# Kernel tuning notes

Measured on AMD Instinct MI355X. Metric: run time of the kernel, lower is better.

The kernel has to match this reference:

```python
import jax, jax.numpy as jnp
import numpy as np

ALPHA = 1.702
LIMIT = 7.0


def setup_inputs() -> dict:
    key = jax.random.key(0)
    ks = jax.random.split(key, 6)
    T, H, D, E = 8192, 1024, 1024, 8
    hidden_states = jax.random.normal(ks[0], (T, H), dtype=jnp.float32)
    routing_weights = jax.random.uniform(ks[1], (T, E), dtype=jnp.float32)
    # 0.02 scale keeps activations in a sane range (original uses raw randn params)
    gate_up_proj = jax.random.normal(ks[2], (E, H, 2 * D), dtype=jnp.float32) * 0.02
    gate_up_proj_bias = jax.random.normal(ks[3], (E, 2 * D), dtype=jnp.float32) * 0.02
    down_proj = jax.random.normal(ks[4], (E, D, H), dtype=jnp.float32) * 0.02
    down_proj_bias = jax.random.normal(ks[5], (E, H), dtype=jnp.float32) * 0.02
    return {
        "hidden_states": hidden_states,
        "routing_weights": routing_weights,
        "gate_up_proj": gate_up_proj,
        "gate_up_proj_bias": gate_up_proj_bias,
        "down_proj": down_proj,
        "down_proj_bias": down_proj_bias,
    }


def reference(hidden_states, routing_weights, gate_up_proj, gate_up_proj_bias,
              down_proj, down_proj_bias):
    # hidden_states: [T, H]; routing_weights: [T, E] (batch_size == T in the torch code)
    B, H = hidden_states.shape[0], hidden_states.shape[-1]
    hs = hidden_states.reshape(-1, H)  # [T, H]
    # all-experts batched GEMM: [E, T, 2D]
    gate_up = jnp.einsum('th,ehd->etd', hs, gate_up_proj) + gate_up_proj_bias[:, None, :]
    gate = jnp.minimum(gate_up[..., ::2], LIMIT)          # [E, T, D]
    up = jnp.clip(gate_up[..., 1::2], -LIMIT, LIMIT)      # [E, T, D]
    glu = gate * jax.nn.sigmoid(gate * ALPHA)
    # down projection: [E, T, H]
    next_states = jnp.einsum('etd,edh->eth', (up + 1.0) * glu, down_proj) \
        + down_proj_bias[:, None, :]
    # routing-weighted combine over experts: [T, H]
    out = jnp.einsum('eth,te->th', next_states, routing_weights)
    return out.reshape(B, -1, H)  # [T, 1, H], matching final .view(batch_size, -1, hidden)
```

## Files before the change

### kernel.cpp

```cpp
#include <hip/hip_runtime.h>
#include <hip/hip_bf16.h>

#define T_DIM 8192
#define H_DIM 1024
#define D_DIM 1024
#define E_DIM 8
#define TWO_D 2048
#define K2 8192

#define ALPHA_C 1.702f
#define LIMIT_C 7.0f

typedef __attribute__((ext_vector_type(8))) short s8v;
typedef __attribute__((ext_vector_type(4))) float f4v;

__device__ __forceinline__ void g2l16(const void* g, void* l) {
    __builtin_amdgcn_global_load_lds((const __attribute__((address_space(1))) void*)g,
                                     (__attribute__((address_space(3))) void*)l, 16, 0, 0);
}

__device__ __forceinline__ unsigned short f2bf(float f) {
    __hip_bfloat16 h = __float2bfloat16(f);
    return __builtin_bit_cast(unsigned short, h);
}

__device__ __forceinline__ float bf2f(unsigned short u) {
    unsigned int x = ((unsigned int)u) << 16;
    return __builtin_bit_cast(float, x);
}


__global__ void f32_to_bf16_kernel(const float* __restrict__ in,
                                   unsigned short* __restrict__ out, size_t n) {
    size_t i = ((size_t)blockIdx.x * blockDim.x + threadIdx.x) * 4;
    if (i + 3 < n) {
        float4 v = *(const float4*)(in + i);
        ushort4 o;
        o.x = f2bf(v.x); o.y = f2bf(v.y); o.z = f2bf(v.z); o.w = f2bf(v.w);
        *(ushort4*)(out + i) = o;
    }
}

__global__ void transpose_conv_kernel(const float* __restrict__ in,
                                      unsigned short* __restrict__ out,
                                      int cols, size_t ibs, size_t obs, size_t ors,
                                      int remap) {
    __shared__ float t[32][33];
    const int b = blockIdx.z;
    const int c0 = blockIdx.x * 32, r0 = blockIdx.y * 32;
    const int tx = threadIdx.x & 31, ty = threadIdx.x >> 5;
    const float* ip = in + (size_t)b * ibs;
    #pragma unroll
    for (int i = 0; i < 4; ++i)
        t[ty + i * 8][tx] = ip[(size_t)(r0 + ty + i * 8) * cols + c0 + tx];
    __syncthreads();
    unsigned short* op = out + (size_t)b * obs;
    #pragma unroll
    for (int i = 0; i < 4; ++i) {
        int c = c0 + ty + i * 8;
        int nc = remap ? ((c & ~31) + ((c & 1) << 4) + ((c >> 1) & 15)) : c;
        op[(size_t)nc * ors + r0 + tx] = f2bf(t[tx][ty + i * 8]);
    }
}

__global__ void reduce_bias_kernel(const unsigned short* __restrict__ p0,
                                   const unsigned short* __restrict__ p1,
                                   const unsigned short* __restrict__ p2,
                                   const float* __restrict__ rw,
                                   const float* __restrict__ b3,
                                   float* __restrict__ out) {
    const int t = blockIdx.x;
    const int h = threadIdx.x * 4;
    const size_t idx = (size_t)t * H_DIM + h;
    float r[E_DIM];
    #pragma unroll
    for (int e = 0; e < E_DIM; ++e) r[e] = rw[(size_t)t * E_DIM + e];
    float4 v = *(const float4*)(out + idx);
    ushort4 a = *(const ushort4*)(p0 + idx);
    ushort4 b = *(const ushort4*)(p1 + idx);
    ushort4 c = *(const ushort4*)(p2 + idx);
    v.x += bf2f(a.x) + bf2f(b.x) + bf2f(c.x);
    v.y += bf2f(a.y) + bf2f(b.y) + bf2f(c.y);
    v.z += bf2f(a.z) + bf2f(b.z) + bf2f(c.z);
    v.w += bf2f(a.w) + bf2f(b.w) + bf2f(c.w);
    #pragma unroll
    for (int e = 0; e < E_DIM; ++e) {
        float4 bb = *(const float4*)(b3 + (size_t)e * H_DIM + h);
        v.x += r[e] * bb.x; v.y += r[e] * bb.y; v.z += r[e] * bb.z; v.w += r[e] * bb.w;
    }
    *(float4*)(out + idx) = v;
}


__global__ __launch_bounds__(256, 2) void gemm1_kernel(
    const short* __restrict__ Ag0,
    const short* __restrict__ Bg0,
    const float* __restrict__ b1,
    const float* __restrict__ rw,
    __hip_bfloat16* __restrict__ act2)
{
    const int e = blockIdx.z;
    const int mBase = blockIdx.x * 128;
    const int nBase = blockIdx.y * 128;
    const int tid = threadIdx.x;
    const int lane = tid & 63;
    const int wave = tid >> 6;
    const int wm = wave >> 1, wn = wave & 1;
    const int cq = lane & 15, quad = lane >> 4;

    __shared__ __align__(16) short As[128 * 64];
    __shared__ __align__(16) short Bs[128 * 64];

    const short* Ag = Ag0 + (size_t)mBase * H_DIM;
    const short* Bg = Bg0 + ((size_t)e * TWO_D + nBase) * H_DIM;

    f4v acc[4][4];
    #pragma unroll
    for (int mt = 0; mt < 4; ++mt)
        #pragma unroll
        for (int nt = 0; nt < 4; ++nt)
            acc[mt][nt] = (f4v){0.f, 0.f, 0.f, 0.f};

    const int srow8 = lane >> 3;
    const int gco = ((lane & 7) ^ srow8) * 8;
    const int cq7 = cq & 7;

    for (int k0 = 0; k0 < H_DIM; k0 += 64) {
        #pragma unroll
        for (int i = 0; i < 4; ++i) {
            const int r = wave * 32 + i * 8 + srow8;
            g2l16(Ag + (size_t)r * H_DIM + k0 + gco, As + (wave * 32 + i * 8) * 64);
            g2l16(Bg + (size_t)r * H_DIM + k0 + gco, Bs + (wave * 32 + i * 8) * 64);
        }
        __syncthreads();
        #pragma unroll
        for (int h = 0; h < 2; ++h) {
            s8v af[4], bf[4];
            const int pc = (((h << 2) + quad) ^ cq7) * 8;
            #pragma unroll
            for (int i = 0; i < 4; ++i) {
                af[i] = *(const s8v*)(As + (wm * 64 + i * 16 + cq) * 64 + pc);
                bf[i] = *(const s8v*)(Bs + (wn * 64 + i * 16 + cq) * 64 + pc);
            }
            #pragma unroll
            for (int mt = 0; mt < 4; ++mt)
                #pragma unroll
                for (int nt = 0; nt < 4; ++nt)
                    acc[mt][nt] = __builtin_amdgcn_mfma_f32_16x16x32_bf16(
                        af[mt], bf[nt], acc[mt][nt], 0, 0, 0);
        }
        __syncthreads();
    }

    float rwv[4][4];
    #pragma unroll
    for (int mt = 0; mt < 4; ++mt)
        #pragma unroll
        for (int r = 0; r < 4; ++r)
            rwv[mt][r] = rw[(size_t)(mBase + wm * 64 + mt * 16 + quad * 4 + r) * E_DIM + e];

    #pragma unroll
    for (int p = 0; p < 2; ++p) {
        const int j = (((nBase + wn * 64 + p * 32) >> 5) << 4) + cq;
        const float gb = b1[(size_t)e * TWO_D + 2 * j];
        const float ub = b1[(size_t)e * TWO_D + 2 * j + 1];
        #pragma unroll
        for (int mt = 0; mt < 4; ++mt) {
            #pragma unroll
            for (int r = 0; r < 4; ++r) {
                float gate = acc[mt][2 * p][r] + gb;
                float up   = acc[mt][2 * p + 1][r] + ub;
                gate = fminf(gate, LIMIT_C);
                up = fminf(fmaxf(up, -LIMIT_C), LIMIT_C);
                float glu = gate / (1.f + __expf(-ALPHA_C * gate));
                float a = (up + 1.f) * glu * rwv[mt][r];
                const int row = mBase + wm * 64 + mt * 16 + quad * 4 + r;
                act2[(size_t)row * K2 + (size_t)e * D_DIM + j] = __float2bfloat16(a);
            }
        }
    }
}


#define KSLICE 2048

__global__ __launch_bounds__(256, 2) void gemm2_kernel(
    const short* __restrict__ Ag0,
    const short* __restrict__ Bg0,
    float* __restrict__ out,
    unsigned short* __restrict__ p0,
    unsigned short* __restrict__ p1,
    unsigned short* __restrict__ p2)
{
    const int id = blockIdx.x;
    const int nBase = (id & 7) * 128;
    const int mBase = ((id >> 3) & 63) * 128;
    const int kIdx = id >> 9;
    const int kBase = kIdx * KSLICE;
    const int tid = threadIdx.x;
    const int lane = tid & 63;
    const int wave = tid >> 6;
    const int wm = wave >> 1, wn = wave & 1;
    const int cq = lane & 15, quad = lane >> 4;

    __shared__ __align__(16) short As[128 * 64];
    __shared__ __align__(16) short Bs[128 * 64];

    const short* Ag = Ag0 + (size_t)mBase * K2;
    const short* Bg = Bg0 + (size_t)nBase * K2;

    f4v acc[4][4];
    #pragma unroll
    for (int mt = 0; mt < 4; ++mt)
        #pragma unroll
        for (int nt = 0; nt < 4; ++nt)
            acc[mt][nt] = (f4v){0.f, 0.f, 0.f, 0.f};

    const int srow8 = lane >> 3;
    const int gco = ((lane & 7) ^ srow8) * 8;
    const int cq7 = cq & 7;

    for (int k0 = kBase; k0 < kBase + KSLICE; k0 += 64) {
        #pragma unroll
        for (int i = 0; i < 4; ++i) {
            const int r = wave * 32 + i * 8 + srow8;
            g2l16(Ag + (size_t)r * K2 + k0 + gco, As + (wave * 32 + i * 8) * 64);
            g2l16(Bg + (size_t)r * K2 + k0 + gco, Bs + (wave * 32 + i * 8) * 64);
        }
        __syncthreads();
        #pragma unroll
        for (int h = 0; h < 2; ++h) {
            s8v af[4], bf[4];
            const int pc = (((h << 2) + quad) ^ cq7) * 8;
            #pragma unroll
            for (int i = 0; i < 4; ++i) {
                af[i] = *(const s8v*)(As + (wm * 64 + i * 16 + cq) * 64 + pc);
                bf[i] = *(const s8v*)(Bs + (wn * 64 + i * 16 + cq) * 64 + pc);
            }
            #pragma unroll
            for (int mt = 0; mt < 4; ++mt)
                #pragma unroll
                for (int nt = 0; nt < 4; ++nt)
                    acc[mt][nt] = __builtin_amdgcn_mfma_f32_16x16x32_bf16(
                        af[mt], bf[nt], acc[mt][nt], 0, 0, 0);
        }
        __syncthreads();
    }

    unsigned short* pdst = (kIdx == 1) ? p0 : (kIdx == 2) ? p1 : p2;
    #pragma unroll
    for (int mt = 0; mt < 4; ++mt) {
        #pragma unroll
        for (int r = 0; r < 4; ++r) {
            const int row = mBase + wm * 64 + mt * 16 + quad * 4 + r;
            const size_t idx = (size_t)row * H_DIM + nBase + wn * 64 + 16 * 0 + cq;
            #pragma unroll
            for (int nt = 0; nt < 4; ++nt) {
                const size_t o = (size_t)row * H_DIM + nBase + wn * 64 + nt * 16 + cq;
                if (kIdx == 0) out[o] = acc[mt][nt][r];
                else           pdst[o] = f2bf(acc[mt][nt][r]);
            }
            (void)idx;
        }
    }
}


extern "C" void kernel_launch(void* const* d_in, const int* in_sizes, int n_in,
                              void* d_out, int out_size, void* d_ws, size_t ws_size,
                              hipStream_t stream) {
    const float* hs = (const float*)d_in[0];
    const float* rw = (const float*)d_in[1];
    const float* w1 = (const float*)d_in[2];
    const float* b1 = (const float*)d_in[3];
    const float* w3 = (const float*)d_in[4];
    const float* b3 = (const float*)d_in[5];
    float* out = (float*)d_out;

    char* ws = (char*)d_ws;
    unsigned short* hsb  = (unsigned short*)(ws);
    unsigned short* w1b  = (unsigned short*)(ws + ((size_t)16 << 20));
    unsigned short* w3b  = (unsigned short*)(ws + ((size_t)48 << 20));
    unsigned short* act2 = (unsigned short*)(ws + ((size_t)64 << 20));
    unsigned short* p0 = (unsigned short*)(ws);
    unsigned short* p1 = (unsigned short*)(ws + ((size_t)16 << 20));
    unsigned short* p2 = (unsigned short*)(ws + ((size_t)32 << 20));

    {
        size_t n = (size_t)T_DIM * H_DIM;
        f32_to_bf16_kernel<<<dim3(n / (256 * 4)), dim3(256), 0, stream>>>(hs, hsb, n);
    }
    transpose_conv_kernel<<<dim3(TWO_D / 32, H_DIM / 32, E_DIM), dim3(256), 0, stream>>>(
        w1, w1b, TWO_D, (size_t)H_DIM * TWO_D, (size_t)TWO_D * H_DIM, (size_t)H_DIM, 1);
    transpose_conv_kernel<<<dim3(H_DIM / 32, D_DIM / 32, E_DIM), dim3(256), 0, stream>>>(
        w3, w3b, H_DIM, (size_t)D_DIM * H_DIM, (size_t)D_DIM, (size_t)K2, 0);
    gemm1_kernel<<<dim3(T_DIM / 128, TWO_D / 128, E_DIM), dim3(256), 0, stream>>>(
        (const short*)hsb, (const short*)w1b, b1, rw, (__hip_bfloat16*)act2);
    gemm2_kernel<<<dim3(8 * 64 * 4), dim3(256), 0, stream>>>(
        (const short*)act2, (const short*)w3b, out, p0, p1, p2);
    reduce_bias_kernel<<<dim3(T_DIM), dim3(H_DIM / 4), 0, stream>>>(
        p0, p1, p2, rw, b3, out);
}
```

Before: 628.1 us.

## Use 256x256 tiles with multi-stage LDS pipelined GEMM core and 2-way split-K

```diff
diff --git a/kernel.cpp b/kernel.cpp
--- a/kernel.cpp
+++ b/kernel.cpp
@@ -64,8 +64,6 @@
 }
 
 __global__ void reduce_bias_kernel(const unsigned short* __restrict__ p0,
-                                   const unsigned short* __restrict__ p1,
-                                   const unsigned short* __restrict__ p2,
                                    const float* __restrict__ rw,
                                    const float* __restrict__ b3,
                                    float* __restrict__ out) {
@@ -77,12 +75,10 @@
     for (int e = 0; e < E_DIM; ++e) r[e] = rw[(size_t)t * E_DIM + e];
     float4 v = *(const float4*)(out + idx);
     ushort4 a = *(const ushort4*)(p0 + idx);
-    ushort4 b = *(const ushort4*)(p1 + idx);
-    ushort4 c = *(const ushort4*)(p2 + idx);
-    v.x += bf2f(a.x) + bf2f(b.x) + bf2f(c.x);
-    v.y += bf2f(a.y) + bf2f(b.y) + bf2f(c.y);
-    v.z += bf2f(a.z) + bf2f(b.z) + bf2f(c.z);
-    v.w += bf2f(a.w) + bf2f(b.w) + bf2f(c.w);
+    v.x += bf2f(a.x);
+    v.y += bf2f(a.y);
+    v.z += bf2f(a.z);
+    v.w += bf2f(a.w);
     #pragma unroll
     for (int e = 0; e < E_DIM; ++e) {
         float4 bb = *(const float4*)(b3 + (size_t)e * H_DIM + h);
@@ -92,7 +88,100 @@
 }
 
 
-__global__ __launch_bounds__(256, 2) void gemm1_kernel(
+#define FEN asm volatile("" ::: "memory")
+#define BARR { FEN; __builtin_amdgcn_s_barrier(); FEN; }
+#define LGKM0 asm volatile("s_waitcnt lgkmcnt(0)" ::: "memory")
+
+#define LDA4(BUF, KH, CH)                                                        \
+  { const short* _p = &As[BUF][KH][aoff + (CH) * 2048];                          \
+    a[0] = *(const s8v*)(_p);        a[1] = *(const s8v*)(_p + 512);             \
+    a[2] = *(const s8v*)(_p + 1024); a[3] = *(const s8v*)(_p + 1536); }
+
+#define LDB4(BUF, KH)                                                            \
+  { const short* _p = &Bs[BUF][KH][boff];                                        \
+    b[0] = *(const s8v*)(_p);        b[1] = *(const s8v*)(_p + 512);             \
+    b[2] = *(const s8v*)(_p + 1024); b[3] = *(const s8v*)(_p + 1536); }
+
+#define MM16(CH)                                                                 \
+  { _Pragma("unroll")                                                            \
+    for (int mf = 0; mf < 4; ++mf) {                                             \
+      _Pragma("unroll")                                                          \
+      for (int nf = 0; nf < 4; ++nf)                                             \
+        acc[(CH) * 4 + mf][nf] = __builtin_amdgcn_mfma_f32_16x16x32_bf16(        \
+            a[mf], b[nf], acc[(CH) * 4 + mf][nf], 0, 0, 0);                      \
+    } }
+
+#define STG(GB, SLOT, KEL)                                                       \
+  { const short* _g = (GB) + (size_t)rstage * sK + (KEL) + gco;                  \
+    g2l16(_g, &(SLOT)[wave * 1024]);                                             \
+    g2l16(_g + 16 * sK, &(SLOT)[wave * 1024 + 512]); }
+
+#define PHASE_TAIL(CH)                                                           \
+  BARR; LGKM0;                                                                   \
+  __builtin_amdgcn_s_setprio(1);                                                 \
+  MM16(CH);                                                                      \
+  __builtin_amdgcn_s_setprio(0);                                                 \
+  BARR;
+
+#define TILE(T, BUF)                                                             \
+  { const int _kel = kbase + (T) * 64;                                           \
+    LDA4(BUF, 0, 0); LDB4(BUF, 0);                                               \
+    if ((T) + 1 < NT) STG(Ag, As[(BUF) ^ 1][1], _kel + 96);                      \
+    PHASE_TAIL(0)                                                                \
+    LDA4(BUF, 0, 1);                                                             \
+    if ((T) + 1 < NT) STG(Bg, Bs[(BUF) ^ 1][1], _kel + 96);                      \
+    PHASE_TAIL(1)                                                                \
+    LDA4(BUF, 1, 0); LDB4(BUF, 1);                                               \
+    if ((T) + 2 < NT) STG(Ag, As[BUF][0], _kel + 128);                           \
+    PHASE_TAIL(0)                                                                \
+    LDA4(BUF, 1, 1);                                                             \
+    if ((T) + 2 < NT) STG(Bg, Bs[BUF][0], _kel + 128);                           \
+    if ((T) + 2 < NT) { asm volatile("s_waitcnt vmcnt(4)" ::: "memory"); }       \
+    else              { asm volatile("s_waitcnt vmcnt(0)" ::: "memory"); }       \
+    PHASE_TAIL(1)                                                                \
+  }
+
+__device__ __forceinline__ void gemm_core(const short* __restrict__ Ag,
+                                          const short* __restrict__ Bg,
+                                          const size_t sK, const int kbase,
+                                          const int NT, f4v (&acc)[8][4]) {
+    __shared__ __align__(16) short As[2][2][8192];
+    __shared__ __align__(16) short Bs[2][2][8192];
+    const int tid = threadIdx.x;
+    const int lane = tid & 63;
+    const int wave = tid >> 6;
+    const int wm = wave >> 2, wn = wave & 3;
+    const int cq = lane & 15, quad = lane >> 4;
+    const int gco = (((lane & 3) ^ ((lane >> 3) & 3)) << 3);
+    const int rstage = wave * 32 + (lane >> 2);
+    const int rc = ((quad ^ ((cq >> 1) & 3)) << 3);
+    const int aoff = wm * 4096 + cq * 32 + rc;
+    const int boff = wn * 2048 + cq * 32 + rc;
+
+    s8v a[4], b[4];
+    #pragma unroll
+    for (int i = 0; i < 8; ++i)
+        #pragma unroll
+        for (int j = 0; j < 4; ++j) acc[i][j] = (f4v){0.f, 0.f, 0.f, 0.f};
+
+    STG(Ag, As[0][0], kbase);
+    STG(Bg, Bs[0][0], kbase);
+    STG(Ag, As[0][1], kbase + 32);
+    STG(Bg, Bs[0][1], kbase + 32);
+    STG(Ag, As[1][0], kbase + 64);
+    STG(Bg, Bs[1][0], kbase + 64);
+    asm volatile("s_waitcnt vmcnt(4)" ::: "memory");
+    BARR;
+
+    #pragma unroll 1
+    for (int t = 0; t < NT; t += 2) {
+        TILE(t, 0)
+        TILE(t + 1, 1)
+    }
+}
+
+
+__global__ __launch_bounds__(512, 2) void gemm1_kernel(
     const short* __restrict__ Ag0,
     const short* __restrict__ Bg0,
     const float* __restrict__ b1,
@@ -100,64 +189,17 @@
     __hip_bfloat16* __restrict__ act2)
 {
     const int e = blockIdx.z;
-    const int mBase = blockIdx.x * 128;
-    const int nBase = blockIdx.y * 128;
-    const int tid = threadIdx.x;
-    const int lane = tid & 63;
-    const int wave = tid >> 6;
-    const int wm = wave >> 1, wn = wave & 1;
-    const int cq = lane & 15, quad = lane >> 4;
-
-    __shared__ __align__(16) short As[128 * 64];
-    __shared__ __align__(16) short Bs[128 * 64];
-
+    const int mBase = blockIdx.x * 256;
+    const int nBase = blockIdx.y * 256;
     const short* Ag = Ag0 + (size_t)mBase * H_DIM;
     const short* Bg = Bg0 + ((size_t)e * TWO_D + nBase) * H_DIM;
 
-    f4v acc[4][4];
-    #pragma unroll
-    for (int mt = 0; mt < 4; ++mt)
-        #pragma unroll
-        for (int nt = 0; nt < 4; ++nt)
-            acc[mt][nt] = (f4v){0.f, 0.f, 0.f, 0.f};
-
-    const int srow8 = lane >> 3;
-    const int gco = ((lane & 7) ^ srow8) * 8;
-    const int cq7 = cq & 7;
-
-    for (int k0 = 0; k0 < H_DIM; k0 += 64) {
-        #pragma unroll
-        for (int i = 0; i < 4; ++i) {
-            const int r = wave * 32 + i * 8 + srow8;
-            g2l16(Ag + (size_t)r * H_DIM + k0 + gco, As + (wave * 32 + i * 8) * 64);
-            g2l16(Bg + (size_t)r * H_DIM + k0 + gco, Bs + (wave * 32 + i * 8) * 64);
-        }
-        __syncthreads();
-        #pragma unroll
-        for (int h = 0; h < 2; ++h) {
-            s8v af[4], bf[4];
-            const int pc = (((h << 2) + quad) ^ cq7) * 8;
-            #pragma unroll
-            for (int i = 0; i < 4; ++i) {
-                af[i] = *(const s8v*)(As + (wm * 64 + i * 16 + cq) * 64 + pc);
-                bf[i] = *(const s8v*)(Bs + (wn * 64 + i * 16 + cq) * 64 + pc);
-            }
-            #pragma unroll
-            for (int mt = 0; mt < 4; ++mt)
-                #pragma unroll
-                for (int nt = 0; nt < 4; ++nt)
-                    acc[mt][nt] = __builtin_amdgcn_mfma_f32_16x16x32_bf16(
-                        af[mt], bf[nt], acc[mt][nt], 0, 0, 0);
-        }
-        __syncthreads();
-    }
-
-    float rwv[4][4];
-    #pragma unroll
-    for (int mt = 0; mt < 4; ++mt)
-        #pragma unroll
-        for (int r = 0; r < 4; ++r)
-            rwv[mt][r] = rw[(size_t)(mBase + wm * 64 + mt * 16 + quad * 4 + r) * E_DIM + e];
+    f4v acc[8][4];
+    gemm_core(Ag, Bg, H_DIM, 0, H_DIM / 64, acc);
+
+    const int lane = threadIdx.x & 63, wave = threadIdx.x >> 6;
+    const int wm = wave >> 2, wn = wave & 3;
+    const int cq = lane & 15, quad = lane >> 4;
 
     #pragma unroll
     for (int p = 0; p < 2; ++p) {
@@ -165,102 +207,55 @@
         const float gb = b1[(size_t)e * TWO_D + 2 * j];
         const float ub = b1[(size_t)e * TWO_D + 2 * j + 1];
         #pragma unroll
-        for (int mt = 0; mt < 4; ++mt) {
+        for (int fm = 0; fm < 8; ++fm) {
             #pragma unroll
             for (int r = 0; r < 4; ++r) {
-                float gate = acc[mt][2 * p][r] + gb;
-                float up   = acc[mt][2 * p + 1][r] + ub;
+                const int row = mBase + wm * 128 + fm * 16 + quad * 4 + r;
+                const float rwv = rw[(size_t)row * E_DIM + e];
+                float gate = acc[fm][2 * p][r] + gb;
+                float up   = acc[fm][2 * p + 1][r] + ub;
                 gate = fminf(gate, LIMIT_C);
                 up = fminf(fmaxf(up, -LIMIT_C), LIMIT_C);
                 float glu = gate / (1.f + __expf(-ALPHA_C * gate));
-                float a = (up + 1.f) * glu * rwv[mt][r];
-                const int row = mBase + wm * 64 + mt * 16 + quad * 4 + r;
-                act2[(size_t)row * K2 + (size_t)e * D_DIM + j] = __float2bfloat16(a);
+                float av = (up + 1.f) * glu * rwv;
+                act2[(size_t)row * K2 + (size_t)e * D_DIM + j] = __float2bfloat16(av);
             }
         }
     }
 }
 
 
-#define KSLICE 2048
-
-__global__ __launch_bounds__(256, 2) void gemm2_kernel(
+__global__ __launch_bounds__(512, 2) void gemm2_kernel(
     const short* __restrict__ Ag0,
     const short* __restrict__ Bg0,
     float* __restrict__ out,
-    unsigned short* __restrict__ p0,
-    unsigned short* __restrict__ p1,
-    unsigned short* __restrict__ p2)
+    unsigned short* __restrict__ p0)
 {
     const int id = blockIdx.x;
-    const int nBase = (id & 7) * 128;
-    const int mBase = ((id >> 3) & 63) * 128;
-    const int kIdx = id >> 9;
-    const int kBase = kIdx * KSLICE;
-    const int tid = threadIdx.x;
-    const int lane = tid & 63;
-    const int wave = tid >> 6;
-    const int wm = wave >> 1, wn = wave & 1;
-    const int cq = lane & 15, quad = lane >> 4;
-
-    __shared__ __align__(16) short As[128 * 64];
-    __shared__ __align__(16) short Bs[128 * 64];
-
+    const int nBase = (id & 3) * 256;
+    const int mBase = ((id >> 2) & 31) * 256;
+    const int kIdx = id >> 7;
     const short* Ag = Ag0 + (size_t)mBase * K2;
     const short* Bg = Bg0 + (size_t)nBase * K2;
 
-    f4v acc[4][4];
-    #pragma unroll
-    for (int mt = 0; mt < 4; ++mt)
-        #pragma unroll
-        for (int nt = 0; nt < 4; ++nt)
-            acc[mt][nt] = (f4v){0.f, 0.f, 0.f, 0.f};
-
-    const int srow8 = lane >> 3;
-    const int gco = ((lane & 7) ^ srow8) * 8;
-    const int cq7 = cq & 7;
-
-    for (int k0 = kBase; k0 < kBase + KSLICE; k0 += 64) {
-        #pragma unroll
-        for (int i = 0; i < 4; ++i) {
-            const int r = wave * 32 + i * 8 + srow8;
-            g2l16(Ag + (size_t)r * K2 + k0 + gco, As + (wave * 32 + i * 8) * 64);
-            g2l16(Bg + (size_t)r * K2 + k0 + gco, Bs + (wave * 32 + i * 8) * 64);
-        }
-        __syncthreads();
-        #pragma unroll
-        for (int h = 0; h < 2; ++h) {
-            s8v af[4], bf[4];
-            const int pc = (((h << 2) + quad) ^ cq7) * 8;
-            #pragma unroll
-            for (int i = 0; i < 4; ++i) {
-                af[i] = *(const s8v*)(As + (wm * 64 + i * 16 + cq) * 64 + pc);
-                bf[i] = *(const s8v*)(Bs + (wn * 64 + i * 16 + cq) * 64 + pc);
-            }
-            #pragma unroll
-            for (int mt = 0; mt < 4; ++mt)
-                #pragma unroll
-                for (int nt = 0; nt < 4; ++nt)
-                    acc[mt][nt] = __builtin_amdgcn_mfma_f32_16x16x32_bf16(
-                        af[mt], bf[nt], acc[mt][nt], 0, 0, 0);
-        }
-        __syncthreads();
-    }
-
-    unsigned short* pdst = (kIdx == 1) ? p0 : (kIdx == 2) ? p1 : p2;
-    #pragma unroll
-    for (int mt = 0; mt < 4; ++mt) {
+    f4v acc[8][4];
+    gemm_core(Ag, Bg, K2, kIdx * 4096, 4096 / 64, acc);
+
+    const int lane = threadIdx.x & 63, wave = threadIdx.x >> 6;
+    const int wm = wave >> 2, wn = wave & 3;
+    const int cq = lane & 15, quad = lane >> 4;
+
+    #pragma unroll
+    for (int fm = 0; fm < 8; ++fm) {
         #pragma unroll
         for (int r = 0; r < 4; ++r) {
-            const int row = mBase + wm * 64 + mt * 16 + quad * 4 + r;
-            const size_t idx = (size_t)row * H_DIM + nBase + wn * 64 + 16 * 0 + cq;
+            const int row = mBase + wm * 128 + fm * 16 + quad * 4 + r;
             #pragma unroll
-            for (int nt = 0; nt < 4; ++nt) {
-                const size_t o = (size_t)row * H_DIM + nBase + wn * 64 + nt * 16 + cq;
-                if (kIdx == 0) out[o] = acc[mt][nt][r];
-                else           pdst[o] = f2bf(acc[mt][nt][r]);
+            for (int nf = 0; nf < 4; ++nf) {
+                const size_t o = (size_t)row * H_DIM + nBase + wn * 64 + nf * 16 + cq;
+                if (kIdx == 0) out[o] = acc[fm][nf][r];
+                else           p0[o]  = f2bf(acc[fm][nf][r]);
             }
-            (void)idx;
         }
     }
 }
@@ -283,8 +278,6 @@
     unsigned short* w3b  = (unsigned short*)(ws + ((size_t)48 << 20));
     unsigned short* act2 = (unsigned short*)(ws + ((size_t)64 << 20));
     unsigned short* p0 = (unsigned short*)(ws);
-    unsigned short* p1 = (unsigned short*)(ws + ((size_t)16 << 20));
-    unsigned short* p2 = (unsigned short*)(ws + ((size_t)32 << 20));
 
     {
         size_t n = (size_t)T_DIM * H_DIM;
@@ -294,10 +287,10 @@
         w1, w1b, TWO_D, (size_t)H_DIM * TWO_D, (size_t)TWO_D * H_DIM, (size_t)H_DIM, 1);
     transpose_conv_kernel<<<dim3(H_DIM / 32, D_DIM / 32, E_DIM), dim3(256), 0, stream>>>(
         w3, w3b, H_DIM, (size_t)D_DIM * H_DIM, (size_t)D_DIM, (size_t)K2, 0);
-    gemm1_kernel<<<dim3(T_DIM / 128, TWO_D / 128, E_DIM), dim3(256), 0, stream>>>(
+    gemm1_kernel<<<dim3(T_DIM / 256, TWO_D / 256, E_DIM), dim3(512), 0, stream>>>(
         (const short*)hsb, (const short*)w1b, b1, rw, (__hip_bfloat16*)act2);
-    gemm2_kernel<<<dim3(8 * 64 * 4), dim3(256), 0, stream>>>(
-        (const short*)act2, (const short*)w3b, out, p0, p1, p2);
+    gemm2_kernel<<<dim3(256), dim3(512), 0, stream>>>(
+        (const short*)act2, (const short*)w3b, out, p0);
     reduce_bias_kernel<<<dim3(T_DIM), dim3(H_DIM / 4), 0, stream>>>(
-        p0, p1, p2, rw, b3, out);
-}
+        p0, rw, b3, out);
+}
```

Result: no change. 638.8 us (+1.7%).

## Drop split-K in down-projection GEMM and fuse bias combine into epilogue

Applied to the files above, without the earlier changes.

```diff
diff --git a/kernel.cpp b/kernel.cpp
--- a/kernel.cpp
+++ b/kernel.cpp
@@ -22,11 +22,6 @@
 __device__ __forceinline__ unsigned short f2bf(float f) {
     __hip_bfloat16 h = __float2bfloat16(f);
     return __builtin_bit_cast(unsigned short, h);
-}
-
-__device__ __forceinline__ float bf2f(unsigned short u) {
-    unsigned int x = ((unsigned int)u) << 16;
-    return __builtin_bit_cast(float, x);
 }
 
 
@@ -61,34 +56,6 @@
         int nc = remap ? ((c & ~31) + ((c & 1) << 4) + ((c >> 1) & 15)) : c;
         op[(size_t)nc * ors + r0 + tx] = f2bf(t[tx][ty + i * 8]);
     }
-}
-
-__global__ void reduce_bias_kernel(const unsigned short* __restrict__ p0,
-                                   const unsigned short* __restrict__ p1,
-                                   const unsigned short* __restrict__ p2,
-                                   const float* __restrict__ rw,
-                                   const float* __restrict__ b3,
-                                   float* __restrict__ out) {
-    const int t = blockIdx.x;
-    const int h = threadIdx.x * 4;
-    const size_t idx = (size_t)t * H_DIM + h;
-    float r[E_DIM];
-    #pragma unroll
-    for (int e = 0; e < E_DIM; ++e) r[e] = rw[(size_t)t * E_DIM + e];
-    float4 v = *(const float4*)(out + idx);
-    ushort4 a = *(const ushort4*)(p0 + idx);
-    ushort4 b = *(const ushort4*)(p1 + idx);
-    ushort4 c = *(const ushort4*)(p2 + idx);
-    v.x += bf2f(a.x) + bf2f(b.x) + bf2f(c.x);
-    v.y += bf2f(a.y) + bf2f(b.y) + bf2f(c.y);
-    v.z += bf2f(a.z) + bf2f(b.z) + bf2f(c.z);
-    v.w += bf2f(a.w) + bf2f(b.w) + bf2f(c.w);
-    #pragma unroll
-    for (int e = 0; e < E_DIM; ++e) {
-        float4 bb = *(const float4*)(b3 + (size_t)e * H_DIM + h);
-        v.x += r[e] * bb.x; v.y += r[e] * bb.y; v.z += r[e] * bb.z; v.w += r[e] * bb.w;
-    }
-    *(float4*)(out + idx) = v;
 }
 
 
@@ -182,21 +149,16 @@
 }
 
 
-#define KSLICE 2048
-
 __global__ __launch_bounds__(256, 2) void gemm2_kernel(
     const short* __restrict__ Ag0,
     const short* __restrict__ Bg0,
-    float* __restrict__ out,
-    unsigned short* __restrict__ p0,
-    unsigned short* __restrict__ p1,
-    unsigned short* __restrict__ p2)
+    const float* __restrict__ rw,
+    const float* __restrict__ b3,
+    float* __restrict__ out)
 {
     const int id = blockIdx.x;
     const int nBase = (id & 7) * 128;
-    const int mBase = ((id >> 3) & 63) * 128;
-    const int kIdx = id >> 9;
-    const int kBase = kIdx * KSLICE;
+    const int mBase = (id >> 3) * 128;
     const int tid = threadIdx.x;
     const int lane = tid & 63;
     const int wave = tid >> 6;
@@ -220,7 +182,7 @@
     const int gco = ((lane & 7) ^ srow8) * 8;
     const int cq7 = cq & 7;
 
-    for (int k0 = kBase; k0 < kBase + KSLICE; k0 += 64) {
+    for (int k0 = 0; k0 < K2; k0 += 64) {
         #pragma unroll
         for (int i = 0; i < 4; ++i) {
             const int r = wave * 32 + i * 8 + srow8;
@@ -247,20 +209,22 @@
         __syncthreads();
     }
 
-    unsigned short* pdst = (kIdx == 1) ? p0 : (kIdx == 2) ? p1 : p2;
     #pragma unroll
     for (int mt = 0; mt < 4; ++mt) {
         #pragma unroll
         for (int r = 0; r < 4; ++r) {
             const int row = mBase + wm * 64 + mt * 16 + quad * 4 + r;
-            const size_t idx = (size_t)row * H_DIM + nBase + wn * 64 + 16 * 0 + cq;
+            const float4 rwa = *(const float4*)(rw + (size_t)row * E_DIM);
+            const float4 rwb = *(const float4*)(rw + (size_t)row * E_DIM + 4);
             #pragma unroll
             for (int nt = 0; nt < 4; ++nt) {
-                const size_t o = (size_t)row * H_DIM + nBase + wn * 64 + nt * 16 + cq;
-                if (kIdx == 0) out[o] = acc[mt][nt][r];
-                else           pdst[o] = f2bf(acc[mt][nt][r]);
-            }
-            (void)idx;
+                const int col = nBase + wn * 64 + nt * 16 + cq;
+                float bias = rwa.x * b3[0 * H_DIM + col] + rwa.y * b3[1 * H_DIM + col]
+                           + rwa.z * b3[2 * H_DIM + col] + rwa.w * b3[3 * H_DIM + col]
+                           + rwb.x * b3[4 * H_DIM + col] + rwb.y * b3[5 * H_DIM + col]
+                           + rwb.z * b3[6 * H_DIM + col] + rwb.w * b3[7 * H_DIM + col];
+                out[(size_t)row * H_DIM + col] = acc[mt][nt][r] + bias;
+            }
         }
     }
 }
@@ -282,9 +246,6 @@
     unsigned short* w1b  = (unsigned short*)(ws + ((size_t)16 << 20));
     unsigned short* w3b  = (unsigned short*)(ws + ((size_t)48 << 20));
     unsigned short* act2 = (unsigned short*)(ws + ((size_t)64 << 20));
-    unsigned short* p0 = (unsigned short*)(ws);
-    unsigned short* p1 = (unsigned short*)(ws + ((size_t)16 << 20));
-    unsigned short* p2 = (unsigned short*)(ws + ((size_t)32 << 20));
 
     {
         size_t n = (size_t)T_DIM * H_DIM;
@@ -296,8 +257,6 @@
         w3, w3b, H_DIM, (size_t)D_DIM * H_DIM, (size_t)D_DIM, (size_t)K2, 0);
     gemm1_kernel<<<dim3(T_DIM / 128, TWO_D / 128, E_DIM), dim3(256), 0, stream>>>(
         (const short*)hsb, (const short*)w1b, b1, rw, (__hip_bfloat16*)act2);
-    gemm2_kernel<<<dim3(8 * 64 * 4), dim3(256), 0, stream>>>(
-        (const short*)act2, (const short*)w3b, out, p0, p1, p2);
-    reduce_bias_kernel<<<dim3(T_DIM), dim3(H_DIM / 4), 0, stream>>>(
-        p0, p1, p2, rw, b3, out);
-}
+    gemm2_kernel<<<dim3(512), dim3(256), 0, stream>>>(
+        (const short*)act2, (const short*)w3b, rw, b3, out);
+}
```

Result: faster. 607.2 us (-3.3%).
